# Kernel optimization log

Measured on AMD Instinct MI355X. Metric: run time of the kernel, lower is better.

Reference implementation:

```python
import jax, jax.numpy as jnp
import numpy as np

V = 50257   # vocab
E = 256     # embedding dim
H = 256     # hidden size
NUM_UTT = 256
L = 128     # tokens per utterance (fixed-length stand-in for EOS-split ragged batch)


def setup_inputs() -> dict:
    key = jax.random.key(0)
    ks = jax.random.split(key, 16)
    w = lambda k, shape: (jax.random.normal(k, shape, jnp.float32) * 0.05)
    inp = {
        "utterances_idc": jax.random.randint(ks[0], (NUM_UTT, L), 0, V),
        "emb": w(ks[1], (V, E)),
    }
    i = 2
    for l, din in [(0, E), (1, 2 * H)]:
        for d in "fb":
            inp[f"w_ih{l}{d}"] = w(ks[i], (4 * H, din)); i += 1
            inp[f"w_hh{l}{d}"] = w(ks[i], (4 * H, H)); i += 1
            inp[f"b{l}{d}"] = w(ks[i], (4 * H,)); i += 1  # b_ih + b_hh fused
    return inp


def _lstm_dir(x_tbd, w_ih, w_hh, b):
    # x_tbd: [T, B, Din]; PyTorch gate order i, f, g, o
    T, B, _ = x_tbd.shape
    Hh = w_hh.shape[1]
    def step(carry, xt):
        h, c = carry
        g = xt @ w_ih.T + h @ w_hh.T + b
        i, f, gg, o = jnp.split(g, 4, axis=-1)
        c = jax.nn.sigmoid(f) * c + jax.nn.sigmoid(i) * jnp.tanh(gg)
        h = jax.nn.sigmoid(o) * jnp.tanh(c)
        return (h, c), h
    z = jnp.zeros((B, Hh), x_tbd.dtype)
    _, ys = jax.lax.scan(step, (z, z), x_tbd)
    return ys  # [T, B, Hh]


def _bilstm(x, wf, whf, bf, wb, whb, bb):
    yf = _lstm_dir(x, wf, whf, bf)
    yb = _lstm_dir(x[::-1], wb, whb, bb)[::-1]
    return jnp.concatenate([yf, yb], -1)  # [T, B, 2H]


def reference(utterances_idc, emb,
              w_ih0f, w_hh0f, b0f, w_ih0b, w_hh0b, b0b,
              w_ih1f, w_hh1f, b1f, w_ih1b, w_hh1b, b1b):
    # Batched equivalent of: per-utterance embedding lookup + biLSTM, keep
    # last-timestep output of final layer, concat over utterances.
    x = emb[utterances_idc]                 # [B, T, E]
    x = jnp.transpose(x, (1, 0, 2))         # [T, B, E] (seq-first like batch_first=False)
    x = _bilstm(x, w_ih0f, w_hh0f, b0f, w_ih0b, w_hh0b, b0b)
    x = _bilstm(x, w_ih1f, w_hh1f, b1f, w_ih1b, w_hh1b, b1b)
    return x[-1]                            # [B, 2H] == torch.cat(results, 0)
```

## Files before the change

kernel.cpp:

```cpp
#include <hip/hip_runtime.h>
#include <hip/hip_bf16.h>
#include <hip/hip_fp16.h>


typedef short s8v __attribute__((ext_vector_type(8)));
typedef float f4v __attribute__((ext_vector_type(4)));
typedef unsigned short u16v8 __attribute__((ext_vector_type(8)));

__device__ inline unsigned short f2bf(float x) {
  union { float f; unsigned u; } v; v.f = x;
  unsigned r = v.u + 0x7fffu + ((v.u >> 16) & 1u);
  return (unsigned short)(r >> 16);
}

__device__ inline void gload_lds16(const void* g, void* l) {
  __builtin_amdgcn_global_load_lds((const __attribute__((address_space(1))) unsigned int*)g,
                                   (__attribute__((address_space(3))) unsigned int*)l,
                                   16, 0, 0);
}

__device__ inline float sigm(float x) { return 1.f / (1.f + __expf(-x)); }
__device__ inline float tanh_f(float x) {
  float e = __expf(2.f * x);
  return 1.f - 2.f / (e + 1.f);
}

__global__ __launch_bounds__(256) void embed_kernel(
    const int* __restrict__ idc, const float* __restrict__ emb,
    unsigned short* __restrict__ x0)
{
  int e = (blockIdx.x * 256 + threadIdx.x) * 8;
  int m = e >> 8;
  int col = e & 255;
  int t = m >> 8, b = m & 255;
  int idx = idc[b * 128 + t];
  const float* src = emb + (size_t)idx * 256 + col;
  float4 lo = *(const float4*)src;
  float4 hi = *(const float4*)(src + 4);
  u16v8 o;
  o[0]=f2bf(lo.x); o[1]=f2bf(lo.y); o[2]=f2bf(lo.z); o[3]=f2bf(lo.w);
  o[4]=f2bf(hi.x); o[5]=f2bf(hi.y); o[6]=f2bf(hi.z); o[7]=f2bf(hi.w);
  *(u16v8*)(x0 + e) = o;
}

__global__ __launch_bounds__(256) void pack2_bf16(unsigned short* __restrict__ dst,
    const float* __restrict__ s0, const float* __restrict__ s1, int n_each)
{
  int i = (blockIdx.x * 256 + threadIdx.x) * 4;
  const float* s = (i < n_each) ? (s0 + i) : (s1 + (i - n_each));
  float4 v = *(const float4*)s;
  dst[i] = f2bf(v.x); dst[i+1] = f2bf(v.y); dst[i+2] = f2bf(v.z); dst[i+3] = f2bf(v.w);
}

__global__ __launch_bounds__(256) void pack2_f32(float* __restrict__ dst,
    const float* __restrict__ s0, const float* __restrict__ s1, int n_each)
{
  int i = blockIdx.x * 256 + threadIdx.x;
  dst[i] = (i < n_each) ? s0[i] : s1[i - n_each];
}

__global__ __launch_bounds__(256) void pack_whh(short* __restrict__ dst,
                                                const float* __restrict__ w)
{
  int tid = blockIdx.x * 256 + threadIdx.x;
  int nt = tid >> 9, ks = (tid >> 6) & 7, l = tid & 63;
  const float* src = w + (size_t)(nt*16 + (l & 15))*256 + ks*32 + (l >> 4)*8;
  float4 a = *(const float4*)src;
  float4 b = *(const float4*)(src + 4);
  s8v o;
  o[0]=(short)f2bf(a.x); o[1]=(short)f2bf(a.y); o[2]=(short)f2bf(a.z); o[3]=(short)f2bf(a.w);
  o[4]=(short)f2bf(b.x); o[5]=(short)f2bf(b.y); o[6]=(short)f2bf(b.z); o[7]=(short)f2bf(b.w);
  *(s8v*)(dst + (size_t)tid*8) = o;
}

__global__ __launch_bounds__(256, 2) void gemm_bt(
    const unsigned short* __restrict__ A, const unsigned short* __restrict__ W,
    const float* __restrict__ bias, _Float16* __restrict__ Gout, int K)
{
  __shared__ char lds[65536];
  const int tid = threadIdx.x, l = tid & 63, w = tid >> 6;
  const int m0 = blockIdx.x * 128, n0 = blockIdx.y * 128;
  const int wr = w >> 1, wc = w & 1;
  const int NK = K >> 6;
  const int c15 = l & 15, ld4 = l >> 4;

  f4v acc[4][4];
  #pragma unroll
  for (int i = 0; i < 4; ++i)
    #pragma unroll
    for (int j = 0; j < 4; ++j) acc[i][j] = (f4v){0.f,0.f,0.f,0.f};

  auto stage = [&](int kt, int buf) {
    char* base = lds + buf*32768;
    const unsigned short* As = A + (size_t)m0*K + kt*64;
    const unsigned short* Ws = W + (size_t)n0*K + kt*64;
    int rr8 = l >> 3;
    int sl = (l & 7) ^ rr8;
    #pragma unroll
    for (int j = 0; j < 4; ++j) {
      int rb = (w*4 + j)*8;
      gload_lds16(As + (size_t)(rb + rr8)*K + sl*8, base + (w*4+j)*1024);
      gload_lds16(Ws + (size_t)(rb + rr8)*K + sl*8, base + 16384 + (w*4+j)*1024);
    }
  };

  stage(0, 0);
  __syncthreads();
  for (int kt = 0; kt < NK; ++kt) {
    const int cur = kt & 1;
    if (kt + 1 < NK) stage(kt+1, cur^1);
    const char* ab = lds + cur*32768;
    const char* bb = ab + 16384;
    #pragma unroll
    for (int ks = 0; ks < 2; ++ks) {
      s8v af[4], bf[4];
      #pragma unroll
      for (int mt = 0; mt < 4; ++mt) {
        int row = wr*64 + mt*16 + c15;
        int cb = ks*64 + ld4*16;
        af[mt] = *(const s8v*)(ab + row*128 + (cb ^ ((row & 7) << 4)));
      }
      #pragma unroll
      for (int nt = 0; nt < 4; ++nt) {
        int row = wc*64 + nt*16 + c15;
        int cb = ks*64 + ld4*16;
        bf[nt] = *(const s8v*)(bb + row*128 + (cb ^ ((row & 7) << 4)));
      }
      #pragma unroll
      for (int mt = 0; mt < 4; ++mt)
        #pragma unroll
        for (int nt = 0; nt < 4; ++nt)
          acc[mt][nt] = __builtin_amdgcn_mfma_f32_16x16x32_bf16(af[mt], bf[nt], acc[mt][nt], 0, 0, 0);
    }
    __syncthreads();
  }
  #pragma unroll
  for (int nt = 0; nt < 4; ++nt) {
    int n = n0 + wc*64 + nt*16 + c15;
    float bv = bias[n];
    #pragma unroll
    for (int mt = 0; mt < 4; ++mt) {
      int mb = m0 + wr*64 + mt*16 + ld4*4;
      #pragma unroll
      for (int j = 0; j < 4; ++j)
        Gout[(size_t)(mb + j)*2048 + n] = (_Float16)(acc[mt][nt][j] + bv);
    }
  }
}

__global__ __launch_bounds__(512, 1) void scan_kernel(
    const _Float16* __restrict__ G,
    const short* __restrict__ whhF, const short* __restrict__ whhB,
    unsigned short* __restrict__ hexch, int hstride,
    float* __restrict__ fout,
    int* __restrict__ flags, int T)
{
  __shared__ char lds[147456];
  char* wlds = lds;
  char* gbuf = lds + 131072;

  const int tid = threadIdx.x;
  const int l = tid & 63;
  const int w = tid >> 6;
  const int ds = blockIdx.x;
  const int dir = blockIdx.y;
  const int q = blockIdx.z;
  const int b0 = ds * 32;
  const int hcol = dir * 256;
  const short* __restrict__ whh = dir ? whhB : whhF;
  int* cnt = flags + (dir*8 + ds) * T;
  const int ld4 = l >> 4;
  const int c15 = l & 15;
  const int s = w >> 2;
  const int u = w & 3;

  #pragma unroll
  for (int j = 0; j < 16; ++j) {
    int idx2 = w*16 + j;
    int g = idx2 >> 5, rem = idx2 & 31, uu = rem >> 3, ks = rem & 7;
    int nt = g*16 + q*4 + uu;
    gload_lds16(whh + ((size_t)(nt*8 + ks)*64 + l)*8, wlds + idx2*1024);
  }

  float cst[4];
  #pragma unroll
  for (int i = 0; i < 4; ++i) cst[i] = 0.f;

  for (int t = 0; t < T; ++t) {
    const int teff = dir ? (T - 1 - t) : t;

    #pragma unroll
    for (int j = 0; j < 2; ++j) {
      const char* gsrc = (const char*)(G +
          ((size_t)(teff*256 + b0 + s*16 + j*8 + (l >> 3)))*2048 +
          dir*1024 + (size_t)(u*256 + q*64)) + (l & 7)*16;
      gload_lds16(gsrc, gbuf + s*8192 + u*2048 + j*1024);
    }

    if (t > 0 && tid == 0) {
      while (__hip_atomic_load(cnt + (t-1), __ATOMIC_ACQUIRE,
                               __HIP_MEMORY_SCOPE_AGENT) < 4) {}
    }
    __syncthreads();

    f4v acc[4];
    #pragma unroll
    for (int i = 0; i < 4; ++i) acc[i] = (f4v){0.f,0.f,0.f,0.f};

    if (t > 0) {
      const int tprev = dir ? (T - t) : (t - 1);
      s8v a[8];
      const unsigned short* hp = hexch +
          ((size_t)tprev*256 + b0 + s*16 + c15)*hstride + hcol + ld4*8;
      #pragma unroll
      for (int ks = 0; ks < 8; ++ks) a[ks] = *(const s8v*)(hp + ks*32);
      #pragma unroll
      for (int g = 0; g < 4; ++g)
        #pragma unroll
        for (int ks = 0; ks < 8; ++ks) {
          s8v b = *(const s8v*)(wlds + ((size_t)((g*4 + u)*8 + ks))*1024 + l*16);
          acc[g] = __builtin_amdgcn_mfma_f32_16x16x32_bf16(a[ks], b, acc[g], 0, 0, 0);
        }
    }

    const bool last = (t == T - 1);
    const int hd = q*64 + u*16 + c15;
    #pragma unroll
    for (int r = 0; r < 4; ++r) {
      const int row = ld4*4 + r;
      const char* gp = gbuf + s*8192 + row*128 + (u*16 + c15)*2;
      float pi = acc[0][r] + (float)*(const _Float16*)(gp);
      float pf = acc[1][r] + (float)*(const _Float16*)(gp + 2048);
      float pg = acc[2][r] + (float)*(const _Float16*)(gp + 4096);
      float po = acc[3][r] + (float)*(const _Float16*)(gp + 6144);
      float cn = sigm(pf) * cst[r] + sigm(pi) * tanh_f(pg);
      cst[r] = cn;
      float hv = sigm(po) * tanh_f(cn);
      const int grow = b0 + s*16 + row;
      hexch[((size_t)teff*256 + grow)*hstride + hcol + hd] = f2bf(hv);
      if (fout && last) fout[grow*512 + hd] = hv;
    }
    __syncthreads();
    if (tid == 0)
      __hip_atomic_fetch_add(cnt + t, 1, __ATOMIC_RELEASE, __HIP_MEMORY_SCOPE_AGENT);
  }
}

__global__ __launch_bounds__(256) void bwd1_kernel(const _Float16* __restrict__ G,
                                                   float* __restrict__ out)
{
  int tid = blockIdx.x * 256 + threadIdx.x;
  int b = tid >> 8, hd = tid & 255;
  const _Float16* g = G + ((size_t)(127*256 + b))*2048 + 1024;
  float pi = (float)g[hd];
  float pg = (float)g[512 + hd];
  float po = (float)g[768 + hd];
  float cn = sigm(pi) * tanh_f(pg);
  out[b*512 + 256 + hd] = sigm(po) * tanh_f(cn);
}

extern "C" void kernel_launch(void* const* d_in, const int* in_sizes, int n_in,
                              void* d_out, int out_size, void* d_ws, size_t ws_size,
                              hipStream_t stream)
{
  (void)in_sizes; (void)n_in; (void)out_size; (void)ws_size;
  const int*   idc   = (const int*)d_in[0];
  const float* emb   = (const float*)d_in[1];
  const float* wih0f = (const float*)d_in[2];
  const float* whh0f = (const float*)d_in[3];
  const float* b0f   = (const float*)d_in[4];
  const float* wih0b = (const float*)d_in[5];
  const float* whh0b = (const float*)d_in[6];
  const float* b0b   = (const float*)d_in[7];
  const float* wih1f = (const float*)d_in[8];
  const float* whh1f = (const float*)d_in[9];
  const float* b1f   = (const float*)d_in[10];
  const float* wih1b = (const float*)d_in[11];
  const float* b1b   = (const float*)d_in[13];

  char* ws = (char*)d_ws;
  unsigned short* X0   = (unsigned short*)(ws);
  unsigned short* Y0   = (unsigned short*)(ws + 16777216);
  _Float16*       Gb   = (_Float16*)(ws + 50331648);
  unsigned short* W0P  = (unsigned short*)(ws + 184549376);
  unsigned short* W1P  = (unsigned short*)(ws + 185597952);
  short*          WH0F = (short*)(ws + 187695104);
  short*          WH0B = (short*)(ws + 188219392);
  short*          WH1F = (short*)(ws + 188743680);
  float*          B0P  = (float*)(ws + 189267968);
  float*          B1P  = (float*)(ws + 189276160);
  int*            FLG0 = (int*)(ws + 189284352);
  int*            FLG1 = (int*)(ws + 189292544);
  float* out = (float*)d_out;

  hipMemsetAsync(ws + 189284352, 0, 12288, stream);

  embed_kernel<<<dim3(4096), dim3(256), 0, stream>>>(idc, emb, X0);
  pack2_bf16<<<dim3(512),  dim3(256), 0, stream>>>(W0P, wih0f, wih0b, 262144);
  pack2_bf16<<<dim3(1024), dim3(256), 0, stream>>>(W1P, wih1f, wih1b, 524288);
  pack2_f32 <<<dim3(8),    dim3(256), 0, stream>>>(B0P, b0f, b0b, 1024);
  pack2_f32 <<<dim3(8),    dim3(256), 0, stream>>>(B1P, b1f, b1b, 1024);
  pack_whh  <<<dim3(128),  dim3(256), 0, stream>>>(WH0F, whh0f);
  pack_whh  <<<dim3(128),  dim3(256), 0, stream>>>(WH0B, whh0b);
  pack_whh  <<<dim3(128),  dim3(256), 0, stream>>>(WH1F, whh1f);

  gemm_bt<<<dim3(256, 16), dim3(256), 0, stream>>>(X0, W0P, B0P, Gb, 256);
  scan_kernel<<<dim3(8, 2, 4), dim3(512), 0, stream>>>(
      Gb, WH0F, WH0B, Y0, 512, (float*)nullptr, FLG0, 128);

  gemm_bt<<<dim3(256, 8), dim3(256), 0, stream>>>(Y0, W1P, B1P, Gb, 512);
  gemm_bt<<<dim3(2, 8), dim3(256), 0, stream>>>(
      Y0 + (size_t)127*256*512, W1P + (size_t)1024*512, B1P + 1024,
      Gb + (size_t)127*256*2048 + 1024, 512);

  scan_kernel<<<dim3(8, 1, 4), dim3(512), 0, stream>>>(
      Gb, WH1F, WH1F, X0, 256, out, FLG1, 128);
  bwd1_kernel<<<dim3(256), dim3(256), 0, stream>>>(Gb, out);
}
```

Before: 1.596 ms.

## Replace per-step flag counters with sentinel-polled hidden-state exchange in scan

The scan kernel no longer waits on per-timestep atomic counters and block-wide barriers. Consumers instead poll the exchanged hidden-state words directly until none equals an all-ones sentinel, and producers publish h through 64-bit release atomic stores staged via LDS. The hidden buffers are memset to 0xFF before each scan, and the gate-preactivation staging layout in LDS is reorganised per warp so no barrier is needed per step. This removes two __syncthreads and a serial flag spin from each recurrence step, at the cost of large extra memsets and a correctness dependence on bf16 h values never matching the sentinel pattern.

Result: slower. 3.770 ms (+136.2%).

```diff
diff --git a/kernel.cpp b/kernel.cpp
--- a/kernel.cpp
+++ b/kernel.cpp
@@ -6,6 +6,8 @@
 typedef short s8v __attribute__((ext_vector_type(8)));
 typedef float f4v __attribute__((ext_vector_type(4)));
 typedef unsigned short u16v8 __attribute__((ext_vector_type(8)));
+
+#define SENT 0xFFFFFFFFFFFFFFFFULL
 
 __device__ inline unsigned short f2bf(float x) {
   union { float f; unsigned u; } v; v.f = x;
@@ -153,11 +155,12 @@
     const short* __restrict__ whhF, const short* __restrict__ whhB,
     unsigned short* __restrict__ hexch, int hstride,
     float* __restrict__ fout,
-    int* __restrict__ flags, int T)
-{
-  __shared__ char lds[147456];
+    int T)
+{
+  __shared__ char lds[151552];
   char* wlds = lds;
-  char* gbuf = lds + 131072;
+  char* gstr = lds + 131072;
+  char* htb  = lds + 147456;
 
   const int tid = threadIdx.x;
   const int l = tid & 63;
@@ -168,7 +171,6 @@
   const int b0 = ds * 32;
   const int hcol = dir * 256;
   const short* __restrict__ whh = dir ? whhB : whhF;
-  int* cnt = flags + (dir*8 + ds) * T;
   const int ld4 = l >> 4;
   const int c15 = l & 15;
   const int s = w >> 2;
@@ -182,6 +184,8 @@
     gload_lds16(whh + ((size_t)(nt*8 + ks)*64 + l)*8, wlds + idx2*1024);
   }
 
+  char* gbase = gstr + (s*4 + u)*2048;
+
   float cst[4];
   #pragma unroll
   for (int i = 0; i < 4; ++i) cst[i] = 0.f;
@@ -191,17 +195,13 @@
 
     #pragma unroll
     for (int j = 0; j < 2; ++j) {
-      const char* gsrc = (const char*)(G +
-          ((size_t)(teff*256 + b0 + s*16 + j*8 + (l >> 3)))*2048 +
-          dir*1024 + (size_t)(u*256 + q*64)) + (l & 7)*16;
-      gload_lds16(gsrc, gbuf + s*8192 + u*2048 + j*1024);
-    }
-
-    if (t > 0 && tid == 0) {
-      while (__hip_atomic_load(cnt + (t-1), __ATOMIC_ACQUIRE,
-                               __HIP_MEMORY_SCOPE_AGENT) < 4) {}
-    }
-    __syncthreads();
+      int g = j*2 + (l & 1);
+      const char* src = (const char*)G +
+          ((size_t)(teff*256 + b0 + s*16 + (l >> 2)))*4096 +
+          dir*2048 + g*512 + q*128 + u*32 + ((l >> 1) & 1)*16;
+      gload_lds16(src, gbase + j*1024);
+    }
+    if (t == 0) __syncthreads();
 
     f4v acc[4];
     #pragma unroll
@@ -209,11 +209,27 @@
 
     if (t > 0) {
       const int tprev = dir ? (T - t) : (t - 1);
+      const unsigned long long* hq = (const unsigned long long*)(hexch +
+          ((size_t)tprev*256 + b0 + s*16 + c15)*hstride + hcol + ld4*8);
+      unsigned long long wd[16];
+      for (;;) {
+        wd[0] = __hip_atomic_load(hq, __ATOMIC_ACQUIRE, __HIP_MEMORY_SCOPE_AGENT);
+        int ok = (wd[0] != SENT);
+        #pragma unroll
+        for (int i = 1; i < 16; ++i) {
+          wd[i] = __hip_atomic_load(hq + (i >> 1)*8 + (i & 1),
+                                    __ATOMIC_RELAXED, __HIP_MEMORY_SCOPE_AGENT);
+          ok &= (wd[i] != SENT);
+        }
+        if (__all(ok)) break;
+      }
       s8v a[8];
-      const unsigned short* hp = hexch +
-          ((size_t)tprev*256 + b0 + s*16 + c15)*hstride + hcol + ld4*8;
-      #pragma unroll
-      for (int ks = 0; ks < 8; ++ks) a[ks] = *(const s8v*)(hp + ks*32);
+      #pragma unroll
+      for (int ks = 0; ks < 8; ++ks) {
+        union { unsigned long long u2[2]; s8v v; } cv;
+        cv.u2[0] = wd[ks*2]; cv.u2[1] = wd[ks*2 + 1];
+        a[ks] = cv.v;
+      }
       #pragma unroll
       for (int g = 0; g < 4; ++g)
         #pragma unroll
@@ -221,28 +237,35 @@
           s8v b = *(const s8v*)(wlds + ((size_t)((g*4 + u)*8 + ks))*1024 + l*16);
           acc[g] = __builtin_amdgcn_mfma_f32_16x16x32_bf16(a[ks], b, acc[g], 0, 0, 0);
         }
+    } else {
     }
 
     const bool last = (t == T - 1);
-    const int hd = q*64 + u*16 + c15;
     #pragma unroll
     for (int r = 0; r < 4; ++r) {
       const int row = ld4*4 + r;
-      const char* gp = gbuf + s*8192 + row*128 + (u*16 + c15)*2;
-      float pi = acc[0][r] + (float)*(const _Float16*)(gp);
-      float pf = acc[1][r] + (float)*(const _Float16*)(gp + 2048);
-      float pg = acc[2][r] + (float)*(const _Float16*)(gp + 4096);
-      float po = acc[3][r] + (float)*(const _Float16*)(gp + 6144);
+      auto gld = [&](int g) -> float {
+        int lp = (row << 2) | (((c15 >> 3) & 1) << 1) | (g & 1);
+        return (float)*(const _Float16*)(gbase + (g >> 1)*1024 + lp*16 + (c15 & 7)*2);
+      };
+      float pi = acc[0][r] + gld(0);
+      float pf = acc[1][r] + gld(1);
+      float pg = acc[2][r] + gld(2);
+      float po = acc[3][r] + gld(3);
       float cn = sigm(pf) * cst[r] + sigm(pi) * tanh_f(pg);
       cst[r] = cn;
       float hv = sigm(po) * tanh_f(cn);
-      const int grow = b0 + s*16 + row;
-      hexch[((size_t)teff*256 + grow)*hstride + hcol + hd] = f2bf(hv);
-      if (fout && last) fout[grow*512 + hd] = hv;
-    }
-    __syncthreads();
-    if (tid == 0)
-      __hip_atomic_fetch_add(cnt + t, 1, __ATOMIC_RELEASE, __HIP_MEMORY_SCOPE_AGENT);
+      *(unsigned short*)(htb + w*512 + row*32 + c15*2) = f2bf(hv);
+      if (fout && last) fout[(b0 + s*16 + row)*512 + q*64 + u*16 + c15] = hv;
+    }
+    {
+      unsigned long long hval = *(const unsigned long long*)
+          (htb + w*512 + (l >> 2)*32 + (l & 3)*8);
+      unsigned long long* dst = (unsigned long long*)(hexch +
+          ((size_t)teff*256 + b0 + s*16 + (l >> 2))*hstride + hcol +
+          q*64 + u*16 + (l & 3)*4);
+      __hip_atomic_store(dst, hval, __ATOMIC_RELEASE, __HIP_MEMORY_SCOPE_AGENT);
+    }
   }
 }
 
@@ -289,11 +312,9 @@
   short*          WH1F = (short*)(ws + 188743680);
   float*          B0P  = (float*)(ws + 189267968);
   float*          B1P  = (float*)(ws + 189276160);
-  int*            FLG0 = (int*)(ws + 189284352);
-  int*            FLG1 = (int*)(ws + 189292544);
   float* out = (float*)d_out;
 
-  hipMemsetAsync(ws + 189284352, 0, 12288, stream);
+  hipMemsetAsync(Y0, 0xFF, 33554432, stream);
 
   embed_kernel<<<dim3(4096), dim3(256), 0, stream>>>(idc, emb, X0);
   pack2_bf16<<<dim3(512),  dim3(256), 0, stream>>>(W0P, wih0f, wih0b, 262144);
@@ -306,7 +327,9 @@
 
   gemm_bt<<<dim3(256, 16), dim3(256), 0, stream>>>(X0, W0P, B0P, Gb, 256);
   scan_kernel<<<dim3(8, 2, 4), dim3(512), 0, stream>>>(
-      Gb, WH0F, WH0B, Y0, 512, (float*)nullptr, FLG0, 128);
+      Gb, WH0F, WH0B, Y0, 512, (float*)nullptr, 128);
+
+  hipMemsetAsync(X0, 0xFF, 16777216, stream);
 
   gemm_bt<<<dim3(256, 8), dim3(256), 0, stream>>>(Y0, W1P, B1P, Gb, 512);
   gemm_bt<<<dim3(2, 8), dim3(256), 0, stream>>>(
@@ -314,6 +337,6 @@
       Gb + (size_t)127*256*2048 + 1024, 512);
 
   scan_kernel<<<dim3(8, 1, 4), dim3(512), 0, stream>>>(
-      Gb, WH1F, WH1F, X0, 256, out, FLG1, 128);
+      Gb, WH1F, WH1F, X0, 256, out, 128);
   bwd1_kernel<<<dim3(256), dim3(256), 0, stream>>>(Gb, out);
 }
```
